# Optimization experiments

Measured on AMD Instinct MI355X. Metric: run time of the kernel, lower is better.

Reference implementation:

```python
import jax, jax.numpy as jnp
import numpy as np

B, N, D, R, H = 8192, 256, 6, 3, 32


def setup_inputs() -> dict:
    key = jax.random.key(0)
    ks = jax.random.split(key, 8)
    neighbor_states = jax.random.normal(ks[0], (B, N, D), dtype=jnp.float32)
    neighbor_roles = jax.random.randint(ks[1], (B, N), 0, R, dtype=jnp.int32)
    neighbor_mask = jax.random.randint(ks[2], (B, N), 0, 2, dtype=jnp.int32).astype(jnp.bool_)
    trust_weights = jax.random.uniform(ks[3], (B, N), dtype=jnp.float32)
    # per-role MLP params: Linear(D,H) -> ReLU -> Linear(H,1)
    s1 = 1.0 / np.sqrt(D)
    s2 = 1.0 / np.sqrt(H)
    W1 = jax.random.uniform(ks[4], (R, D, H), minval=-s1, maxval=s1, dtype=jnp.float32)
    b1 = jax.random.uniform(ks[5], (R, H), minval=-s1, maxval=s1, dtype=jnp.float32)
    W2 = jax.random.uniform(ks[6], (R, H), minval=-s2, maxval=s2, dtype=jnp.float32)
    b2 = jax.random.uniform(ks[7], (R,), minval=-s2, maxval=s2, dtype=jnp.float32)
    return {
        "neighbor_states": neighbor_states,
        "neighbor_roles": neighbor_roles,
        "neighbor_mask": neighbor_mask,
        "trust_weights": trust_weights,
        "W1": W1, "b1": b1, "W2": W2, "b2": b2,
    }


def reference(neighbor_states, neighbor_roles, neighbor_mask, trust_weights, W1, b1, W2, b2):
    maskf = neighbor_mask.astype(jnp.float32)          # [B, N]
    tw = trust_weights * maskf                          # [B, N]
    # per-role attention scores, vectorized over roles: [B, R, N]
    h = jax.nn.relu(jnp.einsum('bnd,rdh->brnh', neighbor_states, W1) + b1[None, :, None, :])
    scores = jnp.einsum('brnh,rh->brn', h, W2) + b2[None, :, None]
    role_mask = (neighbor_roles[:, None, :] == jnp.arange(R)[None, :, None]).astype(jnp.float32) * maskf[:, None, :]
    scores = scores * role_mask                         # NOTE: multiplicative masking, as in original
    m = scores.max(axis=2, keepdims=True)
    e = jnp.exp(scores - m) * role_mask
    aw = e / (e.sum(axis=2, keepdims=True) + 1e-8)      # [B, R, N]
    w = aw * tw[:, None, :]
    ws = jnp.clip(w.sum(axis=2, keepdims=True), 1e-8)   # [B, R, 1]
    mf = jnp.einsum('brn,bnd->brd', w, neighbor_states) / ws  # [B, R, D]
    return mf.reshape(mf.shape[0], R * D)               # concat roles along last dim
```

## Files before the change

kernel.cpp:

```cpp
#include <hip/hip_runtime.h>
#include <math.h>

#define NBATCH 8192
#define NNEI 256
#define NROLE 3
#define NHID 32
#define NDIM 6

typedef float v2f __attribute__((ext_vector_type(2)));

__device__ __forceinline__ float mlp_score(const float x0, const float x1,
                                           const float x2, const float x3,
                                           const float x4, const float x5,
                                           const float* __restrict__ w1,
                                           const float* __restrict__ bb,
                                           const float* __restrict__ w2,
                                           const float b2v) {
  const float x[NDIM] = {x0, x1, x2, x3, x4, x5};
  v2f ac0 = {0.f, 0.f}, ac1 = {0.f, 0.f}, ac2 = {0.f, 0.f}, ac3 = {0.f, 0.f};
#pragma unroll
  for (int h = 0; h < NHID; h += 8) {
    v2f a0 = *(const v2f*)(bb + h + 0);
    v2f a1 = *(const v2f*)(bb + h + 2);
    v2f a2 = *(const v2f*)(bb + h + 4);
    v2f a3 = *(const v2f*)(bb + h + 6);
#pragma unroll
    for (int d = 0; d < NDIM; ++d) {
      const float xv = x[d];
      const v2f xv2 = {xv, xv};
      const float* wc = w1 + d * NHID + h;
      a0 += xv2 * (*(const v2f*)(wc + 0));
      a1 += xv2 * (*(const v2f*)(wc + 2));
      a2 += xv2 * (*(const v2f*)(wc + 4));
      a3 += xv2 * (*(const v2f*)(wc + 6));
    }
    a0.x = fmaxf(a0.x, 0.f); a0.y = fmaxf(a0.y, 0.f);
    a1.x = fmaxf(a1.x, 0.f); a1.y = fmaxf(a1.y, 0.f);
    a2.x = fmaxf(a2.x, 0.f); a2.y = fmaxf(a2.y, 0.f);
    a3.x = fmaxf(a3.x, 0.f); a3.y = fmaxf(a3.y, 0.f);
    ac0 += a0 * (*(const v2f*)(w2 + h + 0));
    ac1 += a1 * (*(const v2f*)(w2 + h + 2));
    ac2 += a2 * (*(const v2f*)(w2 + h + 4));
    ac3 += a3 * (*(const v2f*)(w2 + h + 6));
  }
  const v2f st = (ac0 + ac1) + (ac2 + ac3);
  return b2v + st.x + st.y;
}

__global__ __launch_bounds__(256) void hmf_main(
    const float* __restrict__ states,
    const int* __restrict__ roles,
    const int* __restrict__ maskp,
    const float* __restrict__ trust,
    const float* __restrict__ W1,
    const float* __restrict__ b1,
    const float* __restrict__ W2,
    const float* __restrict__ b2g,
    float* __restrict__ out) {
  const int b = blockIdx.x;
  const int tid = threadIdx.x;
  const int wave = tid >> 6;
  const int lane = tid & 63;

  __shared__ float ssort[NNEI * 12];
  __shared__ int scnt[4][3];

  const size_t rowb = (size_t)b * NNEI;
  const int myrole = roles[rowb + tid];
  const int mymask = maskp[rowb + tid];
  const float mytw = trust[rowb + tid];
  const float* sp = states + rowb * NDIM + (size_t)tid * NDIM;
  const float2 sA = *(const float2*)(sp);
  const float2 sB = *(const float2*)(sp + 2);
  const float2 sC = *(const float2*)(sp + 4);
  const bool active = (mymask != 0);

  unsigned long long bal0 = __ballot(active && (myrole == 0));
  unsigned long long bal1 = __ballot(active && (myrole == 1));
  unsigned long long bal2 = __ballot(active && (myrole == 2));
  if (lane < 3) {
    unsigned long long bb = (lane == 0) ? bal0 : (lane == 1) ? bal1 : bal2;
    scnt[wave][lane] = __popcll(bb);
  }
  __syncthreads();

  int cw[4][3];
#pragma unroll
  for (int w = 0; w < 4; ++w)
#pragma unroll
    for (int r = 0; r < 3; ++r) cw[w][r] = scnt[w][r];
  const int tot0 = cw[0][0] + cw[1][0] + cw[2][0] + cw[3][0];
  const int tot1 = cw[0][1] + cw[1][1] + cw[2][1] + cw[3][1];
  const int tot2 = cw[0][2] + cw[1][2] + cw[2][2] + cw[3][2];
  int basev[3];
  basev[0] = 0; basev[1] = tot0; basev[2] = tot0 + tot1;
  int totv[3] = {tot0, tot1, tot2};

  if (active) {
    unsigned long long mybal = (myrole == 0) ? bal0 : (myrole == 1) ? bal1 : bal2;
    unsigned long long lt = (1ull << lane) - 1ull;
    int rank = __popcll(mybal & lt);
    int wbase = 0;
#pragma unroll
    for (int w = 0; w < 4; ++w)
      if (w < wave) wbase += cw[w][myrole];
    int pos = basev[myrole] + wbase + rank;
    float* dst = ssort + pos * 12;
    *(float4*)dst = make_float4(sA.x, sA.y, sB.x, sB.y);
    *(float2*)(dst + 4) = make_float2(sC.x, sC.y);
    dst[6] = mytw;
  }
  __syncthreads();

  if (wave < 3) {
    const int r = __builtin_amdgcn_readfirstlane(wave);
    const int cnt = __builtin_amdgcn_readfirstlane(totv[r]);
    const int base = __builtin_amdgcn_readfirstlane(basev[r]);
    const float* w1 = W1 + r * (NDIM * NHID);
    const float* bb = b1 + r * NHID;
    const float* w2 = W2 + r * NHID;
    const float b2v = b2g[r];

    float q[8];

    if (cnt <= 64) {
      const bool act = lane < cnt;
      int p = base + lane;
      p = (p > NNEI - 1) ? (NNEI - 1) : p;
      const float* s = ssort + p * 12;
      float4 v4 = *(const float4*)s;
      float2 v2 = *(const float2*)(s + 4);
      float tw = s[6];
      if (!act) {
        v4 = make_float4(0.f, 0.f, 0.f, 0.f);
        v2 = make_float2(0.f, 0.f);
        tw = 0.f;
      }
      const float sc = mlp_score(v4.x, v4.y, v4.z, v4.w, v2.x, v2.y, w1, bb, w2, b2v);
      float cm = act ? sc : -INFINITY;
#pragma unroll
      for (int off = 32; off >= 1; off >>= 1)
        cm = fmaxf(cm, __shfl_xor(cm, off));
      const float mx = fmaxf(cm, 0.f);
      const float e = act ? __expf(sc - mx) : 0.f;
      const float et = e * tw;
      q[0] = e; q[1] = et;
      q[2] = et * v4.x; q[3] = et * v4.y; q[4] = et * v4.z;
      q[5] = et * v4.w; q[6] = et * v2.x; q[7] = et * v2.y;
    } else {
      float m_run = (cnt < NNEI) ? 0.f : -INFINITY;
      float Se = 0.f, Set = 0.f;
      float S0 = 0.f, S1 = 0.f, S2 = 0.f, S3 = 0.f, S4 = 0.f, S5 = 0.f;
      const int nch = (cnt + 63) >> 6;
      for (int c = 0; c < nch; ++c) {
        const int idx = c * 64 + lane;
        const bool act = idx < cnt;
        int p = base + idx;
        p = (p > NNEI - 1) ? (NNEI - 1) : p;
        const float* s = ssort + p * 12;
        float4 v4 = *(const float4*)s;
        float2 v2 = *(const float2*)(s + 4);
        float tw = s[6];
        if (!act) {
          v4 = make_float4(0.f, 0.f, 0.f, 0.f);
          v2 = make_float2(0.f, 0.f);
          tw = 0.f;
        }
        float sc = mlp_score(v4.x, v4.y, v4.z, v4.w, v2.x, v2.y, w1, bb, w2, b2v);
        sc = act ? sc : -INFINITY;
        float cm = sc;
#pragma unroll
        for (int off = 32; off >= 1; off >>= 1)
          cm = fmaxf(cm, __shfl_xor(cm, off));
        const float newm = fmaxf(m_run, cm);
        const float scale = __expf(m_run - newm);
        const float e = act ? __expf(sc - newm) : 0.f;
        const float et = e * tw;
        Se = fmaf(Se, scale, e);
        Set = fmaf(Set, scale, et);
        S0 = fmaf(et, v4.x, S0 * scale);
        S1 = fmaf(et, v4.y, S1 * scale);
        S2 = fmaf(et, v4.z, S2 * scale);
        S3 = fmaf(et, v4.w, S3 * scale);
        S4 = fmaf(et, v2.x, S4 * scale);
        S5 = fmaf(et, v2.y, S5 * scale);
        m_run = newm;
      }
      q[0] = Se; q[1] = Set; q[2] = S0; q[3] = S1;
      q[4] = S2; q[5] = S3; q[6] = S4; q[7] = S5;
    }

#pragma unroll
    for (int i = 0; i < 8; ++i) {
#pragma unroll
      for (int off = 1; off < 64; off <<= 1)
        q[i] += __shfl_xor(q[i], off);
    }
    const float denom = q[0] + 1e-8f;
    const float ws = fmaxf(q[1] / denom, 1e-8f);
    float num = q[2];
    num = (lane == 1) ? q[3] : num;
    num = (lane == 2) ? q[4] : num;
    num = (lane == 3) ? q[5] : num;
    num = (lane == 4) ? q[6] : num;
    num = (lane == 5) ? q[7] : num;
    if (lane < NDIM) {
      out[(size_t)b * (NROLE * NDIM) + r * NDIM + lane] = (num / denom) / ws;
    }
  }
}

extern "C" void kernel_launch(void* const* d_in, const int* in_sizes, int n_in,
                              void* d_out, int out_size, void* d_ws, size_t ws_size,
                              hipStream_t stream) {
  const float* states = (const float*)d_in[0];
  const int* roles = (const int*)d_in[1];
  const int* maskp = (const int*)d_in[2];
  const float* trust = (const float*)d_in[3];
  const float* W1 = (const float*)d_in[4];
  const float* b1 = (const float*)d_in[5];
  const float* W2 = (const float*)d_in[6];
  const float* b2 = (const float*)d_in[7];
  float* out = (float*)d_out;

  hmf_main<<<NBATCH, 256, 0, stream>>>(states, roles, maskp, trust, W1, b1, W2, b2, out);
}
```

Measured before the change: 123.8 us.

## Compact neighbors per wave, drop softmax max shift, transpose final reduction

Result: faster. 120.3 us (-2.8%).

```diff
diff --git a/kernel.cpp b/kernel.cpp
--- a/kernel.cpp
+++ b/kernel.cpp
@@ -6,8 +6,10 @@
 #define NROLE 3
 #define NHID 32
 #define NDIM 6
+#define SSTRIDE 16
 
 typedef float v2f __attribute__((ext_vector_type(2)));
+typedef unsigned long long ull;
 
 __device__ __forceinline__ float mlp_score(const float x0, const float x1,
                                            const float x2, const float x3,
@@ -62,8 +64,8 @@
   const int wave = tid >> 6;
   const int lane = tid & 63;
 
-  __shared__ float ssort[NNEI * 12];
-  __shared__ int scnt[4][3];
+  __shared__ float ssort[NNEI * SSTRIDE];
+  __shared__ int scnt[12];
 
   const size_t rowb = (size_t)b * NNEI;
   const int myrole = roles[rowb + tid];
@@ -75,37 +77,20 @@
   const float2 sC = *(const float2*)(sp + 4);
   const bool active = (mymask != 0);
 
-  unsigned long long bal0 = __ballot(active && (myrole == 0));
-  unsigned long long bal1 = __ballot(active && (myrole == 1));
-  unsigned long long bal2 = __ballot(active && (myrole == 2));
-  if (lane < 3) {
-    unsigned long long bb = (lane == 0) ? bal0 : (lane == 1) ? bal1 : bal2;
-    scnt[wave][lane] = __popcll(bb);
-  }
-  __syncthreads();
-
-  int cw[4][3];
-#pragma unroll
-  for (int w = 0; w < 4; ++w)
-#pragma unroll
-    for (int r = 0; r < 3; ++r) cw[w][r] = scnt[w][r];
-  const int tot0 = cw[0][0] + cw[1][0] + cw[2][0] + cw[3][0];
-  const int tot1 = cw[0][1] + cw[1][1] + cw[2][1] + cw[3][1];
-  const int tot2 = cw[0][2] + cw[1][2] + cw[2][2] + cw[3][2];
-  int basev[3];
-  basev[0] = 0; basev[1] = tot0; basev[2] = tot0 + tot1;
-  int totv[3] = {tot0, tot1, tot2};
+  const ull bal0 = __ballot(active && (myrole == 0));
+  const ull bal1 = __ballot(active && (myrole == 1));
+  const ull bal2 = __ballot(active && (myrole == 2));
+  const int c0 = __popcll(bal0);
+  const int c1 = __popcll(bal1);
+  const int c2 = __popcll(bal2);
+  if (lane < 3) scnt[wave * 3 + lane] = (lane == 0) ? c0 : (lane == 1) ? c1 : c2;
 
   if (active) {
-    unsigned long long mybal = (myrole == 0) ? bal0 : (myrole == 1) ? bal1 : bal2;
-    unsigned long long lt = (1ull << lane) - 1ull;
-    int rank = __popcll(mybal & lt);
-    int wbase = 0;
-#pragma unroll
-    for (int w = 0; w < 4; ++w)
-      if (w < wave) wbase += cw[w][myrole];
-    int pos = basev[myrole] + wbase + rank;
-    float* dst = ssort + pos * 12;
+    const ull mybal = (myrole == 0) ? bal0 : (myrole == 1) ? bal1 : bal2;
+    const int rank = __popcll(mybal & ((1ull << lane) - 1ull));
+    const int pre = ((myrole >= 1) ? c0 : 0) + ((myrole >= 2) ? c1 : 0);
+    const int pos = wave * 64 + pre + rank;
+    float* dst = ssort + pos * SSTRIDE;
     *(float4*)dst = make_float4(sA.x, sA.y, sB.x, sB.y);
     *(float2*)(dst + 4) = make_float2(sC.x, sC.y);
     dst[6] = mytw;
@@ -114,20 +99,40 @@
 
   if (wave < 3) {
     const int r = __builtin_amdgcn_readfirstlane(wave);
-    const int cnt = __builtin_amdgcn_readfirstlane(totv[r]);
-    const int base = __builtin_amdgcn_readfirstlane(basev[r]);
+    int cwv[4], prw[4];
+#pragma unroll
+    for (int w = 0; w < 4; ++w) {
+      const int a0 = scnt[w * 3 + 0];
+      const int a1 = scnt[w * 3 + 1];
+      const int a2 = scnt[w * 3 + 2];
+      const int cv = (r == 0) ? a0 : (r == 1) ? a1 : a2;
+      const int pv = ((r >= 1) ? a0 : 0) + ((r >= 2) ? a1 : 0);
+      cwv[w] = __builtin_amdgcn_readfirstlane(cv);
+      prw[w] = __builtin_amdgcn_readfirstlane(pv);
+    }
+    const int acc0 = cwv[0];
+    const int acc1 = acc0 + cwv[1];
+    const int acc2 = acc1 + cwv[2];
+    const int cnt = acc2 + cwv[3];
+
     const float* w1 = W1 + r * (NDIM * NHID);
     const float* bb = b1 + r * NHID;
     const float* w2 = W2 + r * NHID;
     const float b2v = b2g[r];
 
-    float q[8];
+    float q0, q1, q2, q3, q4, q5, q6, q7;
 
     if (cnt <= 64) {
       const bool act = lane < cnt;
-      int p = base + lane;
-      p = (p > NNEI - 1) ? (NNEI - 1) : p;
-      const float* s = ssort + p * 12;
+      const bool s1 = lane >= acc0;
+      const bool s2 = lane >= acc1;
+      const bool s3 = lane >= acc2;
+      int sub = s1 ? acc0 : 0; sub = s2 ? acc1 : sub; sub = s3 ? acc2 : sub;
+      int wb = s1 ? 64 : 0;    wb = s2 ? 128 : wb;    wb = s3 ? 192 : wb;
+      int pr = s1 ? prw[1] : prw[0]; pr = s2 ? prw[2] : pr; pr = s3 ? prw[3] : pr;
+      int pos = wb + pr + (lane - sub);
+      pos = (pos > NNEI - 1) ? (NNEI - 1) : pos;
+      const float* s = ssort + pos * SSTRIDE;
       float4 v4 = *(const float4*)s;
       float2 v2 = *(const float2*)(s + 4);
       float tw = s[6];
@@ -137,27 +142,27 @@
         tw = 0.f;
       }
       const float sc = mlp_score(v4.x, v4.y, v4.z, v4.w, v2.x, v2.y, w1, bb, w2, b2v);
-      float cm = act ? sc : -INFINITY;
-#pragma unroll
-      for (int off = 32; off >= 1; off >>= 1)
-        cm = fmaxf(cm, __shfl_xor(cm, off));
-      const float mx = fmaxf(cm, 0.f);
-      const float e = act ? __expf(sc - mx) : 0.f;
+      const float e = act ? __expf(sc) : 0.f;
       const float et = e * tw;
-      q[0] = e; q[1] = et;
-      q[2] = et * v4.x; q[3] = et * v4.y; q[4] = et * v4.z;
-      q[5] = et * v4.w; q[6] = et * v2.x; q[7] = et * v2.y;
+      q0 = e; q1 = et;
+      q2 = et * v4.x; q3 = et * v4.y; q4 = et * v4.z;
+      q5 = et * v4.w; q6 = et * v2.x; q7 = et * v2.y;
     } else {
-      float m_run = (cnt < NNEI) ? 0.f : -INFINITY;
-      float Se = 0.f, Set = 0.f;
-      float S0 = 0.f, S1 = 0.f, S2 = 0.f, S3 = 0.f, S4 = 0.f, S5 = 0.f;
+      q0 = q1 = q2 = q3 = q4 = q5 = q6 = q7 = 0.f;
       const int nch = (cnt + 63) >> 6;
       for (int c = 0; c < nch; ++c) {
-        const int idx = c * 64 + lane;
-        const bool act = idx < cnt;
-        int p = base + idx;
-        p = (p > NNEI - 1) ? (NNEI - 1) : p;
-        const float* s = ssort + p * 12;
+        const int jj = c * 64 + lane;
+        const bool act = jj < cnt;
+        const bool s1 = jj >= acc0;
+        const bool s2 = jj >= acc1;
+        const bool s3 = jj >= acc2;
+        int sub = s1 ? acc0 : 0; sub = s2 ? acc1 : sub; sub = s3 ? acc2 : sub;
+        int wb = s1 ? 64 : 0;    wb = s2 ? 128 : wb;    wb = s3 ? 192 : wb;
+        int pr = s1 ? prw[1] : prw[0]; pr = s2 ? prw[2] : pr; pr = s3 ? prw[3] : pr;
+        int pos = wb + pr + (jj - sub);
+        pos = (pos > NNEI - 1) ? (NNEI - 1) : pos;
+        pos = (pos < 0) ? 0 : pos;
+        const float* s = ssort + pos * SSTRIDE;
         float4 v4 = *(const float4*)s;
         float2 v2 = *(const float2*)(s + 4);
         float tw = s[6];
@@ -166,46 +171,41 @@
           v2 = make_float2(0.f, 0.f);
           tw = 0.f;
         }
-        float sc = mlp_score(v4.x, v4.y, v4.z, v4.w, v2.x, v2.y, w1, bb, w2, b2v);
-        sc = act ? sc : -INFINITY;
-        float cm = sc;
-#pragma unroll
-        for (int off = 32; off >= 1; off >>= 1)
-          cm = fmaxf(cm, __shfl_xor(cm, off));
-        const float newm = fmaxf(m_run, cm);
-        const float scale = __expf(m_run - newm);
-        const float e = act ? __expf(sc - newm) : 0.f;
+        const float sc = mlp_score(v4.x, v4.y, v4.z, v4.w, v2.x, v2.y, w1, bb, w2, b2v);
+        const float e = act ? __expf(sc) : 0.f;
         const float et = e * tw;
-        Se = fmaf(Se, scale, e);
-        Set = fmaf(Set, scale, et);
-        S0 = fmaf(et, v4.x, S0 * scale);
-        S1 = fmaf(et, v4.y, S1 * scale);
-        S2 = fmaf(et, v4.z, S2 * scale);
-        S3 = fmaf(et, v4.w, S3 * scale);
-        S4 = fmaf(et, v2.x, S4 * scale);
-        S5 = fmaf(et, v2.y, S5 * scale);
-        m_run = newm;
+        q0 += e; q1 += et;
+        q2 = fmaf(et, v4.x, q2); q3 = fmaf(et, v4.y, q3);
+        q4 = fmaf(et, v4.z, q4); q5 = fmaf(et, v4.w, q5);
+        q6 = fmaf(et, v2.x, q6); q7 = fmaf(et, v2.y, q7);
       }
-      q[0] = Se; q[1] = Set; q[2] = S0; q[3] = S1;
-      q[4] = S2; q[5] = S3; q[6] = S4; q[7] = S5;
-    }
-
-#pragma unroll
-    for (int i = 0; i < 8; ++i) {
-#pragma unroll
-      for (int off = 1; off < 64; off <<= 1)
-        q[i] += __shfl_xor(q[i], off);
-    }
-    const float denom = q[0] + 1e-8f;
-    const float ws = fmaxf(q[1] / denom, 1e-8f);
-    float num = q[2];
-    num = (lane == 1) ? q[3] : num;
-    num = (lane == 2) ? q[4] : num;
-    num = (lane == 3) ? q[5] : num;
-    num = (lane == 4) ? q[6] : num;
-    num = (lane == 5) ? q[7] : num;
-    if (lane < NDIM) {
-      out[(size_t)b * (NROLE * NDIM) + r * NDIM + lane] = (num / denom) / ws;
+    }
+
+#pragma unroll
+    for (int off = 1; off <= 4; off <<= 1) {
+      q0 += __shfl_xor(q0, off); q1 += __shfl_xor(q1, off);
+      q2 += __shfl_xor(q2, off); q3 += __shfl_xor(q3, off);
+      q4 += __shfl_xor(q4, off); q5 += __shfl_xor(q5, off);
+      q6 += __shfl_xor(q6, off); q7 += __shfl_xor(q7, off);
+    }
+    const int g = lane & 7;
+    float myq = q0;
+    myq = (g == 1) ? q1 : myq;
+    myq = (g == 2) ? q2 : myq;
+    myq = (g == 3) ? q3 : myq;
+    myq = (g == 4) ? q4 : myq;
+    myq = (g == 5) ? q5 : myq;
+    myq = (g == 6) ? q6 : myq;
+    myq = (g == 7) ? q7 : myq;
+    myq += __shfl_xor(myq, 8);
+    myq += __shfl_xor(myq, 16);
+    myq += __shfl_xor(myq, 32);
+    const float Se = __shfl(myq, 0);
+    const float Set = __shfl(myq, 1);
+    const float denom = Se + 1e-8f;
+    const float ws = fmaxf(Set / denom, 1e-8f);
+    if (lane >= 2 && lane < 8) {
+      out[(size_t)b * (NROLE * NDIM) + r * NDIM + (lane - 2)] = (myq / denom) / ws;
     }
   }
 }
```
